# Performance work log

Hardware: AMD Instinct MI355X
Metric: run time of the kernel (lower is better)

Reference implementation:

```python
import jax, jax.numpy as jnp
import numpy as np

NEG_SLOPE = 0.2
EPS = 1e-16


def setup_inputs() -> dict:
    key = jax.random.key(0)
    k1, k2, k3, k4, k5 = jax.random.split(key, 5)
    N, E, F_IN, H, C = 100000, 1600000, 128, 4, 32
    x = jax.random.normal(k1, (N, F_IN), dtype=jnp.float32)
    edge_index = jax.random.randint(k2, (2, E), 0, N, dtype=jnp.int64)
    W = jax.random.normal(k3, (F_IN, H * C), dtype=jnp.float32) * (1.0 / np.sqrt(F_IN))
    att_src = jax.random.normal(k4, (H, C), dtype=jnp.float32) * 0.1
    att_dst = jax.random.normal(k5, (H, C), dtype=jnp.float32) * 0.1
    bias = jnp.zeros((H * C,), dtype=jnp.float32)
    return {"x": x, "edge_index": edge_index, "W": W, "att_src": att_src,
            "att_dst": att_dst, "bias": bias}


def reference(x, edge_index, W, att_src, att_dst, bias):
    N = x.shape[0]
    H, C = att_src.shape
    # PyG GATConv default: add self-loops
    loops = jnp.arange(N, dtype=edge_index.dtype)
    src = jnp.concatenate([edge_index[0], loops])  # [E+N]
    dst = jnp.concatenate([edge_index[1], loops])  # [E+N]

    h = (x @ W).reshape(N, H, C)                  # [N,H,C]
    a_src = jnp.einsum('nhc,hc->nh', h, att_src)  # [N,H]
    a_dst = jnp.einsum('nhc,hc->nh', h, att_dst)  # [N,H]

    e = a_src[src] + a_dst[dst]                   # [E',H]
    e = jax.nn.leaky_relu(e, NEG_SLOPE)

    # segment softmax over destination nodes (numerically stable)
    m = jax.ops.segment_max(e, dst, num_segments=N)      # [N,H]
    p = jnp.exp(e - m[dst])                               # [E',H]
    s = jax.ops.segment_sum(p, dst, num_segments=N)       # [N,H]
    alpha = p / (s[dst] + EPS)                             # [E',H]

    msg = h[src] * alpha[:, :, None]                       # [E',H,C]
    out = jax.ops.segment_sum(msg, dst, num_segments=N)   # [N,H,C]
    return out.reshape(N, H * C) + bias
```

## Files before the change

kernel.cpp:

```cpp
#include <hip/hip_runtime.h>
#include <stdint.h>


#define SLOT 64
#define CNTS 16

__device__ __forceinline__ float b2f(unsigned short u) {
    union { unsigned int i; float f; } v; v.i = ((unsigned int)u) << 16; return v.f;
}
__device__ __forceinline__ unsigned short f2b(float f) {
    union { float f; unsigned int i; } v; v.f = f;
    unsigned int i = v.i;
    unsigned int r = (i + 0x7FFFu + ((i >> 16) & 1u)) >> 16;
    return (unsigned short)r;
}

__global__ void k_detect(const int* __restrict__ eidx, const unsigned int* __restrict__ xw,
                         int* flags) {
    __shared__ int nz, bf;
    if (threadIdx.x == 0) { nz = 0; bf = 0; }
    __syncthreads();
    int bad = 0;
    for (int i = threadIdx.x; i < 1024; i += 256)
        if (eidx[2 * i + 1] != 0) bad = 1;
    if (bad) atomicOr(&nz, 1);
    int hits = 0;
    for (int i = threadIdx.x; i < 4096; i += 256) {
        unsigned int e = (xw[i] >> 7) & 0xFFu;
        if (e >= 0x60u && e < 0xA0u) ++hits;
    }
    atomicAdd(&bf, hits);
    __syncthreads();
    if (threadIdx.x == 0) {
        flags[0] = (nz == 0) ? 1 : 0;
        flags[1] = (bf > 3072) ? 1 : 0;
    }
}

__device__ __forceinline__ int edge_at(const int* idx32, const long long* idx64,
                                       int is64, long long pos) {
    return is64 ? (int)idx64[pos] : idx32[pos];
}

__global__ void k_prep(const void* __restrict__ Wv, const void* __restrict__ asv,
                       const void* __restrict__ adv, const void* __restrict__ bv,
                       const int* __restrict__ flags,
                       float* __restrict__ Wf, float* __restrict__ attf ,
                       float* __restrict__ biasf ) {
    int isbf = flags[1];
    int tid = blockIdx.x * 256 + threadIdx.x;
    for (int i = tid; i < 16384; i += gridDim.x * 256)
        Wf[i] = isbf ? b2f(((const unsigned short*)Wv)[i]) : ((const float*)Wv)[i];
    if (blockIdx.x == 0) {
        for (int i = threadIdx.x; i < 128; i += 256) {
            attf[i]       = isbf ? b2f(((const unsigned short*)asv)[i]) : ((const float*)asv)[i];
            attf[128 + i] = isbf ? b2f(((const unsigned short*)adv)[i]) : ((const float*)adv)[i];
            biasf[i]      = isbf ? b2f(((const unsigned short*)bv)[i]) : ((const float*)bv)[i];
        }
    }
}

__global__ __launch_bounds__(256) void k_gemm_scatter(
    const void* __restrict__ xv, const float* __restrict__ Wf,
    const float* __restrict__ attf, const int* __restrict__ flags,
    unsigned short* __restrict__ hbf, float* __restrict__ asf,
    float* __restrict__ adf, int N,
    const int* __restrict__ idx32, const long long* __restrict__ idx64,
    int* __restrict__ cnt, int* __restrict__ esrc, int E, int Gg, int Gs) {
    __shared__ float xs[64 * 128];
    int role = blockIdx.x & 1, rb = blockIdx.x >> 1;
    int tid = threadIdx.x;

    if (role == 1) {
        if (rb >= Gs) return;
        int is64 = flags[0];
        int base = (rb * 256 + tid) * 4;
        if (base + 3 < E) {
            int s0, s1, s2, s3, d0, d1, d2, d3;
            if (is64) {
                s0 = (int)idx64[base];     s1 = (int)idx64[base + 1];
                s2 = (int)idx64[base + 2]; s3 = (int)idx64[base + 3];
                d0 = (int)idx64[(long long)E + base];     d1 = (int)idx64[(long long)E + base + 1];
                d2 = (int)idx64[(long long)E + base + 2]; d3 = (int)idx64[(long long)E + base + 3];
            } else if ((E & 3) == 0) {
                int4 sv = *(const int4*)(idx32 + base);
                int4 dv = *(const int4*)(idx32 + E + base);
                s0 = sv.x; s1 = sv.y; s2 = sv.z; s3 = sv.w;
                d0 = dv.x; d1 = dv.y; d2 = dv.z; d3 = dv.w;
            } else {
                s0 = idx32[base];     s1 = idx32[base + 1];
                s2 = idx32[base + 2]; s3 = idx32[base + 3];
                d0 = idx32[E + base];     d1 = idx32[E + base + 1];
                d2 = idx32[E + base + 2]; d3 = idx32[E + base + 3];
            }
            int p0 = atomicAdd(&cnt[(size_t)d0 * CNTS], 1);
            int p1 = atomicAdd(&cnt[(size_t)d1 * CNTS], 1);
            int p2 = atomicAdd(&cnt[(size_t)d2 * CNTS], 1);
            int p3 = atomicAdd(&cnt[(size_t)d3 * CNTS], 1);
            if (p0 < SLOT) esrc[(size_t)d0 * SLOT + p0] = s0;
            if (p1 < SLOT) esrc[(size_t)d1 * SLOT + p1] = s1;
            if (p2 < SLOT) esrc[(size_t)d2 * SLOT + p2] = s2;
            if (p3 < SLOT) esrc[(size_t)d3 * SLOT + p3] = s3;
        } else {
            for (int e = base; e < E; ++e) {
                int s = edge_at(idx32, idx64, is64, e);
                int d = edge_at(idx32, idx64, is64, (long long)E + e);
                int p = atomicAdd(&cnt[(size_t)d * CNTS], 1);
                if (p < SLOT) esrc[(size_t)d * SLOT + p] = s;
            }
        }
        return;
    }

    if (rb >= Gg) return;
    int r0 = rb * 64;
    int isbf = flags[1];
    if (isbf) {
        const unsigned short* xb = (const unsigned short*)xv;
#pragma unroll
        for (int it = 0; it < 8; ++it) {
            int e = it * 1024 + tid * 4;
            int r = e >> 7, k = e & 127;
            int gr = r0 + r; if (gr >= N) gr = N - 1;
            ushort4 v = *(const ushort4*)(xb + (size_t)gr * 128 + k);
            float4 f; f.x = b2f(v.x); f.y = b2f(v.y); f.z = b2f(v.z); f.w = b2f(v.w);
            *(float4*)(&xs[r * 128 + k]) = f;
        }
    } else {
        const float* xf = (const float*)xv;
#pragma unroll
        for (int it = 0; it < 8; ++it) {
            int e = it * 1024 + tid * 4;
            int r = e >> 7, k = e & 127;
            int gr = r0 + r; if (gr >= N) gr = N - 1;
            *(float4*)(&xs[r * 128 + k]) = *(const float4*)(xf + (size_t)gr * 128 + k);
        }
    }
    __syncthreads();

    int colg = (tid & 31) * 4;
    int rowg = (tid >> 5) * 8;
    float as4[4], ad4[4];
#pragma unroll
    for (int j = 0; j < 4; ++j) {
        as4[j] = attf[colg + j];
        ad4[j] = attf[128 + colg + j];
    }
    float acc[8][4];
#pragma unroll
    for (int r = 0; r < 8; ++r)
#pragma unroll
        for (int j = 0; j < 4; ++j) acc[r][j] = 0.f;

#pragma unroll 2
    for (int k0 = 0; k0 < 128; k0 += 4) {
        float4 w0 = *(const float4*)(Wf + (k0 + 0) * 128 + colg);
        float4 w1 = *(const float4*)(Wf + (k0 + 1) * 128 + colg);
        float4 w2 = *(const float4*)(Wf + (k0 + 2) * 128 + colg);
        float4 w3 = *(const float4*)(Wf + (k0 + 3) * 128 + colg);
#pragma unroll
        for (int r = 0; r < 8; ++r) {
            float4 x4 = *(const float4*)(&xs[(rowg + r) * 128 + k0]);
            acc[r][0] += x4.x * w0.x + x4.y * w1.x + x4.z * w2.x + x4.w * w3.x;
            acc[r][1] += x4.x * w0.y + x4.y * w1.y + x4.z * w2.y + x4.w * w3.y;
            acc[r][2] += x4.x * w0.z + x4.y * w1.z + x4.z * w2.z + x4.w * w3.z;
            acc[r][3] += x4.x * w0.w + x4.y * w1.w + x4.z * w2.w + x4.w * w3.w;
        }
    }

    int hd = colg >> 5;
#pragma unroll
    for (int r = 0; r < 8; ++r) {
        int gr = r0 + rowg + r;
        float s1 = acc[r][0] * as4[0] + acc[r][1] * as4[1] + acc[r][2] * as4[2] + acc[r][3] * as4[3];
        float s2 = acc[r][0] * ad4[0] + acc[r][1] * ad4[1] + acc[r][2] * ad4[2] + acc[r][3] * ad4[3];
#pragma unroll
        for (int m = 1; m < 8; m <<= 1) {
            s1 += __shfl_xor(s1, m);
            s2 += __shfl_xor(s2, m);
        }
        if ((tid & 7) == 0 && gr < N) {
            asf[(size_t)gr * 4 + hd] = s1;
            adf[(size_t)gr * 4 + hd] = s2;
        }
        if (gr < N) {
            ushort4 hv;
            hv.x = f2b(acc[r][0]); hv.y = f2b(acc[r][1]);
            hv.z = f2b(acc[r][2]); hv.w = f2b(acc[r][3]);
            *(ushort4*)(&hbf[(size_t)gr * 128 + colg]) = hv;
        }
    }
}

__global__ __launch_bounds__(256) void k_aggregate(
    const unsigned short* __restrict__ hbf,
    const float* __restrict__ asf, const float* __restrict__ adf,
    const int* __restrict__ cnt, const int* __restrict__ esrc,
    const int* __restrict__ idx32, const long long* __restrict__ idx64,
    const float* __restrict__ biasf, const int* __restrict__ flags,
    void* __restrict__ outv, int N, int E) {
    __shared__ float p_sh_all[4][SLOT * 4];
    __shared__ int   s_sh_all[4][SLOT];
    int wid = threadIdx.x >> 6;
    int lane = threadIdx.x & 63;
    int n = blockIdx.x * 4 + wid;
    if (n >= N) n = N - 1;
    float* p_sh = p_sh_all[wid];
    int*   s_sh = s_sh_all[wid];
    int head = lane >> 4;

    int deg = cnt[(size_t)n * CNTS];
    float4 adv = *(const float4*)(adf + (size_t)n * 4);
    bool fb = (deg > SLOT - 1);

    float p0 = 0.f, p1 = 0.f, p2 = 0.f, p3 = 0.f;
    if (!fb && lane <= deg) {
        int s = (lane == 0) ? n : esrc[(size_t)n * SLOT + lane - 1];
        float4 av = *(const float4*)(asf + (size_t)s * 4);
        float e0 = av.x + adv.x; e0 = fmaxf(e0, 0.2f * e0); p0 = __expf(e0);
        float e1 = av.y + adv.y; e1 = fmaxf(e1, 0.2f * e1); p1 = __expf(e1);
        float e2 = av.z + adv.z; e2 = fmaxf(e2, 0.2f * e2); p2 = __expf(e2);
        float e3 = av.w + adv.w; e3 = fmaxf(e3, 0.2f * e3); p3 = __expf(e3);
        s_sh[lane] = s;
        p_sh[lane * 4 + 0] = p0; p_sh[lane * 4 + 1] = p1;
        p_sh[lane * 4 + 2] = p2; p_sh[lane * 4 + 3] = p3;
    }
    __syncthreads();

    float b0 = biasf[2 * lane], b1 = biasf[2 * lane + 1];
    float a0 = 0.f, a1 = 0.f, invh;

    if (!fb) {
        float ps0 = p0, ps1 = p1, ps2 = p2, ps3 = p3;
#pragma unroll
        for (int m = 1; m < 64; m <<= 1) {
            ps0 += __shfl_xor(ps0, m);
            ps1 += __shfl_xor(ps1, m);
            ps2 += __shfl_xor(ps2, m);
            ps3 += __shfl_xor(ps3, m);
        }
        float den = head == 0 ? ps0 : head == 1 ? ps1 : head == 2 ? ps2 : ps3;
        invh = 1.0f / (den + 1e-16f);

        int tot = deg + 1;
        int i = 0;
        for (; i + 3 < tot; i += 4) {
            int s0 = s_sh[i], s1 = s_sh[i + 1], s2 = s_sh[i + 2], s3 = s_sh[i + 3];
            float q0 = p_sh[i * 4 + head],       q1 = p_sh[(i + 1) * 4 + head];
            float q2 = p_sh[(i + 2) * 4 + head], q3 = p_sh[(i + 3) * 4 + head];
            unsigned int v0 = *(const unsigned int*)(hbf + (size_t)s0 * 128 + 2 * lane);
            unsigned int v1 = *(const unsigned int*)(hbf + (size_t)s1 * 128 + 2 * lane);
            unsigned int v2 = *(const unsigned int*)(hbf + (size_t)s2 * 128 + 2 * lane);
            unsigned int v3 = *(const unsigned int*)(hbf + (size_t)s3 * 128 + 2 * lane);
            a0 += q0 * b2f((unsigned short)v0) + q1 * b2f((unsigned short)v1)
                + q2 * b2f((unsigned short)v2) + q3 * b2f((unsigned short)v3);
            a1 += q0 * b2f((unsigned short)(v0 >> 16)) + q1 * b2f((unsigned short)(v1 >> 16))
                + q2 * b2f((unsigned short)(v2 >> 16)) + q3 * b2f((unsigned short)(v3 >> 16));
        }
        for (; i < tot; ++i) {
            int s0 = s_sh[i];
            float q0 = p_sh[i * 4 + head];
            unsigned int v0 = *(const unsigned int*)(hbf + (size_t)s0 * 128 + 2 * lane);
            a0 += q0 * b2f((unsigned short)v0);
            a1 += q0 * b2f((unsigned short)(v0 >> 16));
        }
    } else {
        int is64 = flags[0];
        float adh = head == 0 ? adv.x : head == 1 ? adv.y : head == 2 ? adv.z : adv.w;
        float den = 0.f;
        {
            float ev = asf[(size_t)n * 4 + head] + adh; ev = fmaxf(ev, 0.2f * ev);
            float p = __expf(ev);
            unsigned int v = *(const unsigned int*)(hbf + (size_t)n * 128 + 2 * lane);
            den += p;
            a0 += p * b2f((unsigned short)v);
            a1 += p * b2f((unsigned short)(v >> 16));
        }
        for (int e = 0; e < E; ++e) {
            int d = edge_at(idx32, idx64, is64, (long long)E + e);
            if (d == n) {
                int s = edge_at(idx32, idx64, is64, e);
                float ev = asf[(size_t)s * 4 + head] + adh; ev = fmaxf(ev, 0.2f * ev);
                float p = __expf(ev);
                unsigned int v = *(const unsigned int*)(hbf + (size_t)s * 128 + 2 * lane);
                den += p;
                a0 += p * b2f((unsigned short)v);
                a1 += p * b2f((unsigned short)(v >> 16));
            }
        }
        invh = 1.0f / (den + 1e-16f);
    }

    a0 = a0 * invh + b0;
    a1 = a1 * invh + b1;
    if (flags[1]) {
        unsigned int pk = (unsigned int)f2b(a0) | ((unsigned int)f2b(a1) << 16);
        ((unsigned int*)outv)[(size_t)n * 64 + lane] = pk;
    } else {
        float2 f2; f2.x = a0; f2.y = a1;
        *(float2*)((float*)outv + (size_t)n * 128 + 2 * lane) = f2;
    }
}

extern "C" void kernel_launch(void* const* d_in, const int* in_sizes, int n_in,
                              void* d_out, int out_size, void* d_ws, size_t ws_size,
                              hipStream_t stream) {
    const void*      xv    = d_in[0];
    const int*       idx32 = (const int*)d_in[1];
    const long long* idx64 = (const long long*)d_in[1];

    int N = in_sizes[0] / 128;
    int E = in_sizes[1] / 2;

    char* ws = (char*)d_ws;
    size_t o = 0;
    auto alloc = [&](size_t bytes) {
        size_t r = o; o += (bytes + 255) & ~(size_t)255; return r;
    };
    unsigned short* hbf = (unsigned short*)(ws + alloc((size_t)N * 128 * 2));
    float* Wf    = (float*)(ws + alloc(16384 * 4));
    float* attf  = (float*)(ws + alloc(256 * 4));
    float* biasf = (float*)(ws + alloc(128 * 4));
    float* asf   = (float*)(ws + alloc((size_t)N * 4 * 4));
    float* adf   = (float*)(ws + alloc((size_t)N * 4 * 4));
    int* cnt     = (int*)(ws + alloc((size_t)N * CNTS * 4));
    int* flags   = (int*)(ws + alloc(256));
    int* esrc    = (int*)(ws + alloc((size_t)N * SLOT * 4));

    int Gg = (N + 63) / 64;
    int Gs = (E / 4 + 255) / 256;
    int G2 = (Gg > Gs ? Gg : Gs);

    k_detect<<<1, 256, 0, stream>>>(idx32, (const unsigned int*)xv, flags);
    k_prep<<<16, 256, 0, stream>>>(d_in[2], d_in[3], d_in[4], d_in[5], flags, Wf, attf, biasf);
    hipMemsetAsync(cnt, 0, (size_t)N * CNTS * 4, stream);
    k_gemm_scatter<<<2 * G2, 256, 0, stream>>>(xv, Wf, attf, flags, hbf, asf, adf, N,
                                               idx32, idx64, cnt, esrc, E, Gg, Gs);
    k_aggregate<<<(N + 3) / 4, 256, 0, stream>>>(hbf, asf, adf, cnt, esrc, idx32, idx64,
                                                 biasf, flags, d_out, N, E);
}
```

Baseline: 301.1 us.

## Compute node projection with split-fp16 MFMA instead of scalar FP32 FMA

Replaces the scalar FP32 x@W loop with MFMA 16x16x32 f16 instructions. Both x and W are split into hi/lo fp16 parts and combined with three MFMAs to keep close to FP32 accuracy. W is pre-transposed and split in the prep kernel, and x tiles are staged in swizzled LDS to avoid bank conflicts. The h output is staged through LDS for coalesced bf16 stores. The main cost is the extra conversion work, and fp16 range limits could hurt accuracy for large values.

```diff
diff --git a/kernel.cpp b/kernel.cpp
--- a/kernel.cpp
+++ b/kernel.cpp
@@ -4,6 +4,9 @@
 
 #define SLOT 64
 #define CNTS 16
+
+typedef __attribute__((ext_vector_type(8))) _Float16 h8;
+typedef __attribute__((ext_vector_type(4))) float    f4x;
 
 __device__ __forceinline__ float b2f(unsigned short u) {
     union { unsigned int i; float f; } v; v.i = ((unsigned int)u) << 16; return v.f;
@@ -13,6 +16,12 @@
     unsigned int i = v.i;
     unsigned int r = (i + 0x7FFFu + ((i >> 16) & 1u)) >> 16;
     return (unsigned short)r;
+}
+__device__ __forceinline__ unsigned short f2h(float f) {
+    union { _Float16 h; unsigned short u; } v; v.h = (_Float16)f; return v.u;
+}
+__device__ __forceinline__ float h2f(unsigned short u) {
+    union { _Float16 h; unsigned short u; } v; v.u = u; return (float)v.h;
 }
 
 __global__ void k_detect(const int* __restrict__ eidx, const unsigned int* __restrict__ xw,
@@ -45,12 +54,19 @@
 __global__ void k_prep(const void* __restrict__ Wv, const void* __restrict__ asv,
                        const void* __restrict__ adv, const void* __restrict__ bv,
                        const int* __restrict__ flags,
-                       float* __restrict__ Wf, float* __restrict__ attf ,
-                       float* __restrict__ biasf ) {
+                       _Float16* __restrict__ Wth, _Float16* __restrict__ Wtl,
+                       float* __restrict__ attf , float* __restrict__ biasf ) {
     int isbf = flags[1];
     int tid = blockIdx.x * 256 + threadIdx.x;
-    for (int i = tid; i < 16384; i += gridDim.x * 256)
-        Wf[i] = isbf ? b2f(((const unsigned short*)Wv)[i]) : ((const float*)Wv)[i];
+    for (int i = tid; i < 16384; i += gridDim.x * 256) {
+        int col = i >> 7, k = i & 127;
+        float w = isbf ? b2f(((const unsigned short*)Wv)[k * 128 + col])
+                       : ((const float*)Wv)[k * 128 + col];
+        unsigned short hi = f2h(w);
+        unsigned short lo = f2h(w - h2f(hi));
+        ((unsigned short*)Wth)[i] = hi;
+        ((unsigned short*)Wtl)[i] = lo;
+    }
     if (blockIdx.x == 0) {
         for (int i = threadIdx.x; i < 128; i += 256) {
             attf[i]       = isbf ? b2f(((const unsigned short*)asv)[i]) : ((const float*)asv)[i];
@@ -61,13 +77,15 @@
 }
 
 __global__ __launch_bounds__(256) void k_gemm_scatter(
-    const void* __restrict__ xv, const float* __restrict__ Wf,
+    const void* __restrict__ xv,
+    const _Float16* __restrict__ Wth, const _Float16* __restrict__ Wtl,
     const float* __restrict__ attf, const int* __restrict__ flags,
     unsigned short* __restrict__ hbf, float* __restrict__ asf,
     float* __restrict__ adf, int N,
     const int* __restrict__ idx32, const long long* __restrict__ idx64,
     int* __restrict__ cnt, int* __restrict__ esrc, int E, int Gg, int Gs) {
-    __shared__ float xs[64 * 128];
+    __shared__ unsigned short xsh[64 * 128];
+    __shared__ unsigned short xsl[64 * 128];
     int role = blockIdx.x & 1, rb = blockIdx.x >> 1;
     int tid = threadIdx.x;
 
@@ -115,80 +133,129 @@
     if (rb >= Gg) return;
     int r0 = rb * 64;
     int isbf = flags[1];
-    if (isbf) {
-        const unsigned short* xb = (const unsigned short*)xv;
-#pragma unroll
-        for (int it = 0; it < 8; ++it) {
-            int e = it * 1024 + tid * 4;
-            int r = e >> 7, k = e & 127;
-            int gr = r0 + r; if (gr >= N) gr = N - 1;
-            ushort4 v = *(const ushort4*)(xb + (size_t)gr * 128 + k);
-            float4 f; f.x = b2f(v.x); f.y = b2f(v.y); f.z = b2f(v.z); f.w = b2f(v.w);
-            *(float4*)(&xs[r * 128 + k]) = f;
-        }
-    } else {
-        const float* xf = (const float*)xv;
-#pragma unroll
-        for (int it = 0; it < 8; ++it) {
-            int e = it * 1024 + tid * 4;
-            int r = e >> 7, k = e & 127;
-            int gr = r0 + r; if (gr >= N) gr = N - 1;
-            *(float4*)(&xs[r * 128 + k]) = *(const float4*)(xf + (size_t)gr * 128 + k);
-        }
-    }
-    __syncthreads();
-
-    int colg = (tid & 31) * 4;
-    int rowg = (tid >> 5) * 8;
-    float as4[4], ad4[4];
-#pragma unroll
-    for (int j = 0; j < 4; ++j) {
-        as4[j] = attf[colg + j];
-        ad4[j] = attf[128 + colg + j];
-    }
-    float acc[8][4];
-#pragma unroll
-    for (int r = 0; r < 8; ++r)
-#pragma unroll
-        for (int j = 0; j < 4; ++j) acc[r][j] = 0.f;
-
-#pragma unroll 2
-    for (int k0 = 0; k0 < 128; k0 += 4) {
-        float4 w0 = *(const float4*)(Wf + (k0 + 0) * 128 + colg);
-        float4 w1 = *(const float4*)(Wf + (k0 + 1) * 128 + colg);
-        float4 w2 = *(const float4*)(Wf + (k0 + 2) * 128 + colg);
-        float4 w3 = *(const float4*)(Wf + (k0 + 3) * 128 + colg);
-#pragma unroll
-        for (int r = 0; r < 8; ++r) {
-            float4 x4 = *(const float4*)(&xs[(rowg + r) * 128 + k0]);
-            acc[r][0] += x4.x * w0.x + x4.y * w1.x + x4.z * w2.x + x4.w * w3.x;
-            acc[r][1] += x4.x * w0.y + x4.y * w1.y + x4.z * w2.y + x4.w * w3.y;
-            acc[r][2] += x4.x * w0.z + x4.y * w1.z + x4.z * w2.z + x4.w * w3.z;
-            acc[r][3] += x4.x * w0.w + x4.y * w1.w + x4.z * w2.w + x4.w * w3.w;
-        }
-    }
-
-    int hd = colg >> 5;
-#pragma unroll
-    for (int r = 0; r < 8; ++r) {
-        int gr = r0 + rowg + r;
-        float s1 = acc[r][0] * as4[0] + acc[r][1] * as4[1] + acc[r][2] * as4[2] + acc[r][3] * as4[3];
-        float s2 = acc[r][0] * ad4[0] + acc[r][1] * ad4[1] + acc[r][2] * ad4[2] + acc[r][3] * ad4[3];
-#pragma unroll
-        for (int m = 1; m < 8; m <<= 1) {
-            s1 += __shfl_xor(s1, m);
-            s2 += __shfl_xor(s2, m);
-        }
-        if ((tid & 7) == 0 && gr < N) {
-            asf[(size_t)gr * 4 + hd] = s1;
-            adf[(size_t)gr * 4 + hd] = s2;
-        }
-        if (gr < N) {
-            ushort4 hv;
-            hv.x = f2b(acc[r][0]); hv.y = f2b(acc[r][1]);
-            hv.z = f2b(acc[r][2]); hv.w = f2b(acc[r][3]);
-            *(ushort4*)(&hbf[(size_t)gr * 128 + colg]) = hv;
-        }
+    int w = tid >> 6;
+    int lane = tid & 63;
+    int li = lane & 15;
+    int g  = lane >> 4;
+    int c0 = w * 32;
+
+    h8 Bh[2][4], Bl[2][4];
+#pragma unroll
+    for (int t = 0; t < 2; ++t)
+#pragma unroll
+        for (int s = 0; s < 4; ++s) {
+            size_t o = (size_t)(c0 + 16 * t + li) * 128 + 32 * s + 8 * g;
+            Bh[t][s] = *(const h8*)(Wth + o);
+            Bl[t][s] = *(const h8*)(Wtl + o);
+        }
+
+#pragma unroll
+    for (int it = 0; it < 4; ++it) {
+        int idx = it * 2048 + tid * 8;
+        int r = idx >> 7, k = idx & 127;
+        int gr = r0 + r; if (gr >= N) gr = N - 1;
+        float v[8];
+        if (isbf) {
+            uint4 raw = *(const uint4*)((const unsigned short*)xv + (size_t)gr * 128 + k);
+            v[0] = b2f((unsigned short)(raw.x & 0xFFFFu)); v[1] = b2f((unsigned short)(raw.x >> 16));
+            v[2] = b2f((unsigned short)(raw.y & 0xFFFFu)); v[3] = b2f((unsigned short)(raw.y >> 16));
+            v[4] = b2f((unsigned short)(raw.z & 0xFFFFu)); v[5] = b2f((unsigned short)(raw.z >> 16));
+            v[6] = b2f((unsigned short)(raw.w & 0xFFFFu)); v[7] = b2f((unsigned short)(raw.w >> 16));
+        } else {
+            const float* xf = (const float*)xv;
+            float4 a = *(const float4*)(xf + (size_t)gr * 128 + k);
+            float4 b = *(const float4*)(xf + (size_t)gr * 128 + k + 4);
+            v[0] = a.x; v[1] = a.y; v[2] = a.z; v[3] = a.w;
+            v[4] = b.x; v[5] = b.y; v[6] = b.z; v[7] = b.w;
+        }
+        uint4 PH, PL;
+        unsigned int ph[4], pl[4];
+#pragma unroll
+        for (int jj = 0; jj < 4; ++jj) {
+            unsigned short h0 = f2h(v[2 * jj]), h1 = f2h(v[2 * jj + 1]);
+            unsigned short l0 = f2h(v[2 * jj] - h2f(h0));
+            unsigned short l1 = f2h(v[2 * jj + 1] - h2f(h1));
+            ph[jj] = (unsigned int)h0 | ((unsigned int)h1 << 16);
+            pl[jj] = (unsigned int)l0 | ((unsigned int)l1 << 16);
+        }
+        PH.x = ph[0]; PH.y = ph[1]; PH.z = ph[2]; PH.w = ph[3];
+        PL.x = pl[0]; PL.y = pl[1]; PL.z = pl[2]; PL.w = pl[3];
+        int off = r * 256 + ((2 * k) ^ ((r & 7) << 4));
+        *(uint4*)((char*)xsh + off) = PH;
+        *(uint4*)((char*)xsl + off) = PL;
+    }
+    __syncthreads();
+
+    f4x acc[4][2];
+#pragma unroll
+    for (int m = 0; m < 4; ++m)
+#pragma unroll
+        for (int t = 0; t < 2; ++t) acc[m][t] = (f4x){0.f, 0.f, 0.f, 0.f};
+
+#pragma unroll
+    for (int s = 0; s < 4; ++s) {
+#pragma unroll
+        for (int m = 0; m < 4; ++m) {
+            int row = 16 * m + li;
+            int kb = (32 * s + 8 * g) * 2;
+            int off = row * 256 + (kb ^ ((row & 7) << 4));
+            h8 ah = *(const h8*)((const char*)xsh + off);
+            h8 al = *(const h8*)((const char*)xsl + off);
+#pragma unroll
+            for (int t = 0; t < 2; ++t) {
+                acc[m][t] = __builtin_amdgcn_mfma_f32_16x16x32_f16(ah, Bh[t][s], acc[m][t], 0, 0, 0);
+                acc[m][t] = __builtin_amdgcn_mfma_f32_16x16x32_f16(al, Bh[t][s], acc[m][t], 0, 0, 0);
+                acc[m][t] = __builtin_amdgcn_mfma_f32_16x16x32_f16(ah, Bl[t][s], acc[m][t], 0, 0, 0);
+            }
+        }
+    }
+
+    float at_s0 = attf[c0 + li],       at_s1 = attf[c0 + 16 + li];
+    float at_d0 = attf[128 + c0 + li], at_d1 = attf[128 + c0 + 16 + li];
+#pragma unroll
+    for (int m = 0; m < 4; ++m) {
+        float s1v[4], s2v[4];
+#pragma unroll
+        for (int j = 0; j < 4; ++j) {
+            s1v[j] = acc[m][0][j] * at_s0 + acc[m][1][j] * at_s1;
+            s2v[j] = acc[m][0][j] * at_d0 + acc[m][1][j] * at_d1;
+        }
+#pragma unroll
+        for (int j = 0; j < 4; ++j) {
+#pragma unroll
+            for (int msk = 1; msk < 16; msk <<= 1) {
+                s1v[j] += __shfl_xor(s1v[j], msk);
+                s2v[j] += __shfl_xor(s2v[j], msk);
+            }
+        }
+        if (li == 0) {
+#pragma unroll
+            for (int j = 0; j < 4; ++j) {
+                int gr = r0 + 16 * m + 4 * g + j;
+                if (gr < N) {
+                    asf[(size_t)gr * 4 + w] = s1v[j];
+                    adf[(size_t)gr * 4 + w] = s2v[j];
+                }
+            }
+        }
+    }
+
+    __syncthreads();
+#pragma unroll
+    for (int m = 0; m < 4; ++m)
+#pragma unroll
+        for (int t = 0; t < 2; ++t)
+#pragma unroll
+            for (int j = 0; j < 4; ++j)
+                xsh[(16 * m + 4 * g + j) * 128 + c0 + 16 * t + li] = f2b(acc[m][t][j]);
+    __syncthreads();
+#pragma unroll
+    for (int it = 0; it < 4; ++it) {
+        int u = it * 2048 + tid * 8;
+        int r = u >> 7, k = u & 127;
+        int gr = r0 + r;
+        if (gr < N)
+            *(uint4*)(hbf + (size_t)gr * 128 + k) = *(const uint4*)(xsh + u);
     }
 }
 
@@ -318,7 +385,8 @@
         size_t r = o; o += (bytes + 255) & ~(size_t)255; return r;
     };
     unsigned short* hbf = (unsigned short*)(ws + alloc((size_t)N * 128 * 2));
-    float* Wf    = (float*)(ws + alloc(16384 * 4));
+    _Float16* Wth = (_Float16*)(ws + alloc(16384 * 2));
+    _Float16* Wtl = (_Float16*)(ws + alloc(16384 * 2));
     float* attf  = (float*)(ws + alloc(256 * 4));
     float* biasf = (float*)(ws + alloc(128 * 4));
     float* asf   = (float*)(ws + alloc((size_t)N * 4 * 4));
@@ -332,9 +400,9 @@
     int G2 = (Gg > Gs ? Gg : Gs);
 
     k_detect<<<1, 256, 0, stream>>>(idx32, (const unsigned int*)xv, flags);
-    k_prep<<<16, 256, 0, stream>>>(d_in[2], d_in[3], d_in[4], d_in[5], flags, Wf, attf, biasf);
+    k_prep<<<16, 256, 0, stream>>>(d_in[2], d_in[3], d_in[4], d_in[5], flags, Wth, Wtl, attf, biasf);
     hipMemsetAsync(cnt, 0, (size_t)N * CNTS * 4, stream);
-    k_gemm_scatter<<<2 * G2, 256, 0, stream>>>(xv, Wf, attf, flags, hbf, asf, adf, N,
+    k_gemm_scatter<<<2 * G2, 256, 0, stream>>>(xv, Wth, Wtl, attf, flags, hbf, asf, adf, N,
                                                idx32, idx64, cnt, esrc, E, Gg, Gs);
     k_aggregate<<<(N + 3) / 4, 256, 0, stream>>>(hbf, asf, adf, cnt, esrc, idx32, idx64,
                                                  biasf, flags, d_out, N, E);
```

Result: faster. 281.3 us (-6.6%).
